# Optimization experiments

Hardware: AMD Instinct MI355X
Metric: run time of the kernel (lower is better)

Reference implementation:

```python
import jax, jax.numpy as jnp
import numpy as np

B, N, C, H, D, K = 8, 2000, 64, 64, 16, 2  # batch, nodes, hidden, hidden_hidden, embed_dim, cheb_k


def setup_inputs() -> dict:
    key = jax.random.key(0)
    ks = jax.random.split(key, 12)
    f = lambda k, s, sc=1.0: jax.random.normal(k, s, dtype=jnp.float32) * sc
    return {
        "z": f(ks[0], (B, N, C)),
        "W_in": f(ks[1], (H, C), 0.1),
        "b_in": f(ks[2], (H,), 0.1),
        "W_out": f(ks[3], (C * C, H), 0.05),
        "b_out": f(ks[4], (C * C,), 0.05),
        "emb": f(ks[5], (N, D), 0.1),
        "wp": f(ks[6], (D, K, H, H), 0.1),
        "bp": f(ks[7], (D, H), 0.1),
        "w1": f(ks[8], (C,)),
        "w2": f(ks[9], (C,)),
        "vs": f(ks[10], (N, N), 0.02),
        "bs": f(ks[11], (N, N), 0.02),
    }


def reference(z, W_in, b_in, W_out, b_out, emb, wp, bp, w1, w2, vs, bs):
    # linear_in + relu: (B,N,C) -> (B,N,H)
    h = jax.nn.relu(jnp.einsum("bnc,hc->bnh", z, W_in) + b_in)

    # data-adaptive graph: softmax over rows of relu(emb @ emb^T)
    A = jax.nn.softmax(jax.nn.relu(emb @ emb.T), axis=1)  # (N,N)
    S = jnp.stack([jnp.eye(N, dtype=z.dtype), A], axis=0)  # (K,N,N), cheb_k=2

    # spatial attention on h (x = h.unsqueeze(1), f_in == H == C)
    e1 = h @ w1  # (B,N)
    e2 = h @ w2  # (B,N)
    prod = e1[:, :, None] * e2[:, None, :]  # (B,N,N) outer product
    E = jax.nn.softmax(
        jnp.einsum("nm,bmp->bnp", vs, jax.nn.sigmoid(prod + bs)), axis=-1
    )  # (B,N,N)

    # batched supports: E.unsqueeze(1) @ S -> (B,K,N,N)
    sup = jnp.einsum("bnm,kmp->bknp", E, S)

    # node-adaptive weights / bias
    weights = jnp.einsum("nd,dkio->nkio", emb, wp)  # (N,K,H,H)
    bias = emb @ bp  # (N,H)

    # graph conv
    x_g = jnp.einsum("bknm,bmc->bnkc", sup, h)  # (B,N,K,H)
    g = jnp.einsum("bnki,nkio->bno", x_g, weights) + bias  # (B,N,H)

    # linear_out + view + tanh, scaled by 0.1
    out = jnp.tanh(jnp.einsum("bnh,oh->bno", g, W_out) + b_out)
    return 0.1 * out.reshape(B, N, C, C)
```

## Files before the change

### kernel.cpp

```cpp
#include <hip/hip_runtime.h>
#include <hip/hip_bf16.h>

#define NN 2000
#define NP 2048
#define BB 8
#define HH 64
#define DD 16

typedef __hip_bfloat16 bf16;
typedef short bf16x8 __attribute__((ext_vector_type(8)));
typedef float f32x4 __attribute__((ext_vector_type(4)));

__device__ __forceinline__ float fast_sigmoid(float x) {
    return 1.0f / (1.0f + __expf(-x));
}
__device__ __forceinline__ float fast_tanh(float x) {
    float e = __expf(2.0f * x);
    return 1.0f - 2.0f / (e + 1.0f);
}

__device__ __forceinline__ void glds16(const void* g, void* l) {
    __builtin_amdgcn_global_load_lds(
        (const __attribute__((address_space(1))) void*)g,
        (__attribute__((address_space(3))) void*)l, 16, 0, 0);
}

__global__ __launch_bounds__(256) void k_h(
        const float* __restrict__ z, const float* __restrict__ W_in,
        const float* __restrict__ b_in, const float* __restrict__ w1,
        const float* __restrict__ w2, float* __restrict__ h,
        float* __restrict__ e1, float* __restrict__ e2) {
    __shared__ float WT[64 * 65];
    __shared__ float zs[4][64];
    int t = threadIdx.x;
    int lane = t & 63, ty = t >> 6;
    int bn0 = blockIdx.x * 4;
    for (int i = t; i < 64 * 64; i += 256) {
        int hh = i >> 6, c = i & 63;
        WT[c * 65 + hh] = W_in[i];
    }
    zs[ty][lane] = z[(size_t)(bn0 + ty) * 64 + lane];
    __syncthreads();
    float acc = b_in[lane];
    #pragma unroll
    for (int c = 0; c < 64; c++) acc += zs[ty][c] * WT[c * 65 + lane];
    float hv = fmaxf(acc, 0.0f);
    h[(size_t)(bn0 + ty) * 64 + lane] = hv;
    float p1 = hv * w1[lane], p2 = hv * w2[lane];
    #pragma unroll
    for (int off = 32; off > 0; off >>= 1) {
        p1 += __shfl_down(p1, off);
        p2 += __shfl_down(p2, off);
    }
    if (lane == 0) { e1[bn0 + ty] = p1; e2[bn0 + ty] = p2; }
}

__global__ __launch_bounds__(256) void k_mega(
        const float* __restrict__ e1, const float* __restrict__ e2,
        const float* __restrict__ bs, bf16* __restrict__ Tt,
        const float* __restrict__ vs, bf16* __restrict__ vs_bf,
        const float* __restrict__ emb, bf16* __restrict__ A,
        const float* __restrict__ wp, float* __restrict__ Wn_all,
        const float* __restrict__ h, bf16* __restrict__ hTcat,
        bf16* __restrict__ hsT,
        const float* __restrict__ W_out, bf16* __restrict__ Wo_bf) {
    __shared__ float smem[4160];
    int bid = blockIdx.x, t = threadIdx.x;

    if (bid < 8192) {
        int b = bid >> 10, rem = bid & 1023;
        int mt = rem & 31, pt = rem >> 5;
        const float* e1b = e1 + (size_t)b * NN;
        const float* e2b = e2 + (size_t)b * NN;
        bf16* Tb = Tt + (size_t)b * NP * NP;
        float* tile = smem;
        int tx = t & 63, ty = t >> 6;
        int m0 = mt * 64, p0 = pt * 64;
        int p = p0 + tx;
        float e2v = (p < NN) ? e2b[p] : 0.0f;
        for (int i = ty * 16; i < ty * 16 + 16; i++) {
            int m = m0 + i;
            float v = 0.0f;
            if (m < NN && p < NN)
                v = fast_sigmoid(e1b[m] * e2v + bs[(size_t)m * NN + p]);
            tile[i * 65 + tx] = v;
        }
        __syncthreads();
        for (int i = ty * 16; i < ty * 16 + 16; i++)
            Tb[((size_t)p0 + i) * NP + m0 + tx] =
                __float2bfloat16(tile[tx * 65 + i]);
        return;
    }
    bid -= 8192;
    if (bid < 16384) {
        int id = bid * 256 + t;
        int n = id >> 11, m = id & (NP - 1);
        float v = (n < NN && m < NN) ? vs[n * NN + m] : 0.0f;
        vs_bf[id] = __float2bfloat16(v);
        return;
    }
    bid -= 16384;
    if (bid < 2048) {
        int i = bid;
        if (i >= NN) {
            for (int j = t; j < NP; j += 256) A[(size_t)i * NP + j] = __float2bfloat16(0.0f);
            return;
        }
        float* rowbuf = smem;
        float* red = smem + 2048;
        float* ei = smem + 2304;
        if (t < DD) ei[t] = emb[i * DD + t];
        __syncthreads();
        float lmax = -1e30f;
        for (int j = t; j < NP; j += 256) {
            float s = 0.0f;
            if (j < NN) {
                #pragma unroll
                for (int d = 0; d < DD; d++) s += ei[d] * emb[j * DD + d];
                s = fmaxf(s, 0.0f);
                lmax = fmaxf(lmax, s);
            }
            rowbuf[j] = s;
        }
        red[t] = lmax; __syncthreads();
        for (int o = 128; o > 0; o >>= 1) { if (t < o) red[t] = fmaxf(red[t], red[t + o]); __syncthreads(); }
        float mx = red[0];
        __syncthreads();
        float lsum = 0.0f;
        for (int j = t; j < NN; j += 256) {
            float e = __expf(rowbuf[j] - mx);
            rowbuf[j] = e; lsum += e;
        }
        red[t] = lsum; __syncthreads();
        for (int o = 128; o > 0; o >>= 1) { if (t < o) red[t] += red[t + o]; __syncthreads(); }
        float inv = 1.0f / red[0];
        for (int j = t; j < NP; j += 256)
            A[(size_t)i * NP + j] = __float2bfloat16(j < NN ? rowbuf[j] * inv : 0.0f);
        return;
    }
    bid -= 2048;
    if (bid < 512) {
        float* embs = smem;
        int n0 = (bid & 15) * 128;
        int jo = (bid >> 4) * 256 + t;
        float wv[16];
        #pragma unroll
        for (int d = 0; d < 16; d++) wv[d] = wp[(size_t)d * 8192 + jo];
        for (int s = t; s < 128 * 16; s += 256) {
            int i = s >> 4, d = s & 15;
            int n = n0 + i;
            embs[s] = (n < NN) ? emb[n * 16 + d] : 0.f;
        }
        __syncthreads();
        for (int i = 0; i < 128; i++) {
            int n = n0 + i;
            if (n >= NN) break;
            const f32x4* ev = (const f32x4*)&embs[i * 16];
            f32x4 ea = ev[0], eb = ev[1], ec = ev[2], ed = ev[3];
            float a = 0.f;
            #pragma unroll
            for (int q = 0; q < 4; q++) a += ea[q] * wv[q];
            #pragma unroll
            for (int q = 0; q < 4; q++) a += eb[q] * wv[4 + q];
            #pragma unroll
            for (int q = 0; q < 4; q++) a += ec[q] * wv[8 + q];
            #pragma unroll
            for (int q = 0; q < 4; q++) a += ed[q] * wv[12 + q];
            Wn_all[(size_t)n * 8192 + jo] = a;
        }
        return;
    }
    bid -= 512;
    if (bid < 256) {
        float* tile = smem;
        int nt = bid & 31, b = bid >> 5;
        int tx = t & 63, ty = t >> 6;
        int n0 = nt * 64;
        for (int i = ty * 16; i < ty * 16 + 16; i++) {
            int n = n0 + i;
            tile[i * 65 + tx] = (n < NN) ? h[((size_t)b * NN + n) * 64 + tx] : 0.0f;
        }
        __syncthreads();
        for (int i = ty * 16; i < ty * 16 + 16; i++) {
            bf16 v = __float2bfloat16(tile[tx * 65 + i]);
            hTcat[((size_t)b * 64 + i) * NP + n0 + tx] = v;
            hsT[((size_t)b * 128 + i) * NP + n0 + tx] = v;
        }
        return;
    }
    bid -= 256;
    {
        int id = bid * 256 + t;
        Wo_bf[id] = __float2bfloat16(W_out[id]);
    }
}

__global__ __launch_bounds__(256) void k_redT(const float* __restrict__ AhPart,
                                              bf16* __restrict__ hsT) {
    __shared__ float tile[64 * 65];
    int pt = blockIdx.x, b = blockIdx.y;
    int tx = threadIdx.x & 63, ty = threadIdx.x >> 6;
    int p0 = pt * 64, q0 = b * 64;
    const long long TOT = (long long)NP * 512;
    for (int i = ty * 16; i < ty * 16 + 16; i++) {
        long long base = ((long long)p0 + i) * 512 + q0 + tx;
        float s = AhPart[base];
        #pragma unroll
        for (int sl = 1; sl < 4; sl++) s += AhPart[sl * TOT + base];
        tile[i * 65 + tx] = s;
    }
    __syncthreads();
    for (int i = ty * 16; i < ty * 16 + 16; i++)
        hsT[((size_t)b * 128 + 64 + i) * NP + p0 + tx] =
            __float2bfloat16(tile[tx * 65 + i]);
}

__global__ __launch_bounds__(512, 4) void k_gemm256pv(
        const bf16* __restrict__ X, const bf16* __restrict__ Yt,
        const bf16* __restrict__ hsT, float* __restrict__ xgPart,
        float* __restrict__ rsPart,
        int K, int ldx, int ldy, long long sY, long long sHs) {
    __shared__ short LDSb[32768];
    short* Asb = LDSb;
    short* Bsb = LDSb + 8192;
    int bx = blockIdx.x, by = blockIdx.y, z = blockIdx.z;
    const bf16* Xp = X;
    const bf16* Yp = Yt + (long long)z * sY;
    int tid = threadIdx.x;
    int m0 = bx * 128, n0 = by * 256;
    int wave = tid >> 6, lane = tid & 63;
    int wr = wave >> 2, wc = wave & 3;
    int fr = lane & 15, kq = lane >> 4;

    f32x4 zero = {0.f, 0.f, 0.f, 0.f};
    f32x4 acc[4][4];
    #pragma unroll
    for (int i = 0; i < 4; i++)
        #pragma unroll
        for (int j = 0; j < 4; j++) acc[i][j] = zero;

    int r4 = tid >> 2, slot = tid & 3;
    int scol = (slot ^ ((r4 >> 1) & 3)) * 8;
    const bf16* xsrc = Xp + (long long)(m0 + r4) * ldx + scol;
    const bf16* ysrc = Yp + (long long)(n0 + r4) * ldy + scol;
    short* Ad = Asb + tid * 8;
    short* Bd = Bsb + tid * 8;

    auto STAGE = [&](int tile) {
        int bufA = (tile & 1) * 4096;
        int bufB = (tile & 1) * 8192;
        long long ko = (long long)tile * 32;
        glds16(xsrc + ko, Ad + bufA);
        glds16(ysrc + ko, Bd + bufB);
        glds16(ysrc + 128 * (long long)ldy + ko, Bd + bufB + 4096);
    };

    int aoff[4], boff[4];
    #pragma unroll
    for (int i = 0; i < 4; i++) {
        int row = wr * 64 + i * 16 + fr;
        aoff[i] = row * 32 + ((kq ^ ((row >> 1) & 3)) << 3);
    }
    #pragma unroll
    for (int j = 0; j < 4; j++) {
        int row = wc * 64 + j * 16 + fr;
        boff[j] = row * 32 + ((kq ^ ((row >> 1) & 3)) << 3);
    }

    int NT = K >> 5;
    STAGE(0); STAGE(1);
    asm volatile("s_waitcnt vmcnt(3)" ::: "memory");
    __builtin_amdgcn_s_barrier();

    for (int t = 0; t < NT; t++) {
        const short* Ab = Asb + (t & 1) * 4096;
        const short* Bb = Bsb + (t & 1) * 8192;
        bf16x8 a[4], b[4];
        #pragma unroll
        for (int i = 0; i < 4; i++) a[i] = *(const bf16x8*)(Ab + aoff[i]);
        #pragma unroll
        for (int j = 0; j < 4; j++) b[j] = *(const bf16x8*)(Bb + boff[j]);
        __builtin_amdgcn_s_setprio(1);
        #pragma unroll
        for (int i = 0; i < 4; i++)
            #pragma unroll
            for (int j = 0; j < 4; j++)
                acc[i][j] = __builtin_amdgcn_mfma_f32_16x16x32_bf16(a[i], b[j], acc[i][j], 0, 0, 0);
        __builtin_amdgcn_s_setprio(0);
        __builtin_amdgcn_sched_barrier(0);
        __builtin_amdgcn_s_barrier();
        __builtin_amdgcn_sched_barrier(0);
        if (t + 2 < NT) {
            STAGE(t + 2);
            asm volatile("s_waitcnt vmcnt(3)" ::: "memory");
        } else if (t + 1 < NT) {
            asm volatile("s_waitcnt vmcnt(0)" ::: "memory");
        }
        __builtin_amdgcn_s_barrier();
    }
    __syncthreads();

    int rq = kq * 4;
    #pragma unroll
    for (int i = 0; i < 4; i++) {
        #pragma unroll
        for (int r = 0; r < 4; r++) {
            int lrow = wr * 64 + i * 16 + rq + r;
            float rs = 0.f;
            #pragma unroll
            for (int j = 0; j < 4; j++) {
                int lcol = wc * 64 + j * 16 + fr;
                float e = (n0 + lcol < NN) ? __expf(acc[i][j][r]) : 0.f;
                bf16 bv = __float2bfloat16(e);
                int sl = (lcol >> 3) ^ (lrow & 7);
                LDSb[lrow * 256 + sl * 8 + (lcol & 7)] = *(short*)&bv;
                rs += e;
            }
            rs += __shfl_xor(rs, 1);
            rs += __shfl_xor(rs, 2);
            rs += __shfl_xor(rs, 4);
            rs += __shfl_xor(rs, 8);
            if (fr == 0)
                rsPart[((long long)z * 32 + by * 4 + wc) * NP + m0 + lrow] = rs;
        }
    }
    __syncthreads();

    const bf16* hz = hsT + (long long)z * sHs;
    int wr2 = wave >> 2, wc2 = wave & 3;
    f32x4 acc2[4][2];
    #pragma unroll
    for (int i = 0; i < 4; i++)
        #pragma unroll
        for (int jj = 0; jj < 2; jj++) acc2[i][jj] = zero;
    #pragma unroll
    for (int ks = 0; ks < 8; ks++) {
        bf16x8 a2[4], b2[2];
        #pragma unroll
        for (int i = 0; i < 4; i++) {
            int row = wr2 * 64 + i * 16 + fr;
            int sl = (ks * 4 + kq) ^ (row & 7);
            a2[i] = *(const bf16x8*)(LDSb + row * 256 + sl * 8);
        }
        #pragma unroll
        for (int jj = 0; jj < 2; jj++)
            b2[jj] = *(const bf16x8*)(hz + (long long)(wc2 * 32 + jj * 16 + fr) * NP
                                      + n0 + ks * 32 + kq * 8);
        #pragma unroll
        for (int i = 0; i < 4; i++)
            #pragma unroll
            for (int jj = 0; jj < 2; jj++)
                acc2[i][jj] = __builtin_amdgcn_mfma_f32_16x16x32_bf16(a2[i], b2[jj], acc2[i][jj], 0, 0, 0);
    }
    #pragma unroll
    for (int i = 0; i < 4; i++)
        #pragma unroll
        for (int jj = 0; jj < 2; jj++) {
            int jcol = wc2 * 32 + jj * 16 + fr;
            #pragma unroll
            for (int r = 0; r < 4; r++) {
                int n = m0 + wr2 * 64 + i * 16 + rq + r;
                xgPart[(long long)n * 8192 + by * 1024 + z * 128 + jcol] = acc2[i][jj][r];
            }
        }
}

template<bool TANH, int KSPLIT>
__global__ __launch_bounds__(256) void k_gemm_bt(
        const bf16* __restrict__ X, const bf16* __restrict__ Yt,
        float* __restrict__ C, const float* __restrict__ bias,
        int K, int ldx, int ldy, int ldc,
        long long sX, long long sY, long long sC, long long sSlice) {
    __shared__ short As[128 * 32];
    __shared__ short Bs[128 * 32];
    int zz = blockIdx.z;
    int ks = 0;
    if (KSPLIT > 1) { ks = zz % KSPLIT; zz /= KSPLIT; }
    const bf16* Xp = X + (long long)zz * sX;
    const bf16* Yp = Yt + (long long)zz * sY;
    float* Cp = C + (long long)zz * sC + (long long)ks * sSlice;
    int tid = threadIdx.x;
    int m0 = blockIdx.x * 128, n0 = blockIdx.y * 128;
    int wave = tid >> 6, lane = tid & 63;
    int wm = (wave >> 1) * 64, wn = (wave & 1) * 64;
    int fr = lane & 15, kq = lane >> 4;

    f32x4 zero = {0.f, 0.f, 0.f, 0.f};
    f32x4 acc[4][4];
    #pragma unroll
    for (int i = 0; i < 4; i++)
        #pragma unroll
        for (int j = 0; j < 4; j++) acc[i][j] = zero;

    int lrow = lane >> 2, lcol = (lane & 3) * 8;
    const bf16* xg0 = Xp + (long long)(m0 + wave * 16 + lrow) * ldx + lcol;
    const bf16* xg1 = xg0 + (long long)64 * ldx;
    const bf16* yg0 = Yp + (long long)(n0 + wave * 16 + lrow) * ldy + lcol;
    const bf16* yg1 = yg0 + (long long)64 * ldy;
    short* lA0 = As + wave * 512;
    short* lA1 = As + (wave + 4) * 512;
    short* lB0 = Bs + wave * 512;
    short* lB1 = Bs + (wave + 4) * 512;

    int kbeg = (KSPLIT > 1) ? ks * (K / KSPLIT) : 0;
    int kend = kbeg + K / KSPLIT;
    for (int k0 = kbeg; k0 < kend; k0 += 32) {
        __syncthreads();
        glds16(xg0 + k0, lA0);
        glds16(xg1 + k0, lA1);
        glds16(yg0 + k0, lB0);
        glds16(yg1 + k0, lB1);
        __syncthreads();
        bf16x8 a[4], b[4];
        #pragma unroll
        for (int i = 0; i < 4; i++)
            a[i] = *(const bf16x8*)(As + (wm + i * 16 + fr) * 32 + kq * 8);
        #pragma unroll
        for (int j = 0; j < 4; j++)
            b[j] = *(const bf16x8*)(Bs + (wn + j * 16 + fr) * 32 + kq * 8);
        #pragma unroll
        for (int i = 0; i < 4; i++)
            #pragma unroll
            for (int j = 0; j < 4; j++)
                acc[i][j] = __builtin_amdgcn_mfma_f32_16x16x32_bf16(a[i], b[j], acc[i][j], 0, 0, 0);
    }
    int rq = kq * 4;
    for (int i = 0; i < 4; i++)
        for (int j = 0; j < 4; j++) {
            int col = n0 + wn + j * 16 + fr;
            float bv = TANH ? bias[col] : 0.0f;
            #pragma unroll
            for (int r = 0; r < 4; r++) {
                int row = m0 + wm + i * 16 + rq + r;
                float v = acc[i][j][r];
                Cp[(long long)row * ldc + col] =
                    TANH ? 0.1f * fast_tanh(v + bv) : v;
            }
        }
}

__global__ __launch_bounds__(256) void k_g(
        const float* __restrict__ Wn_all, const float* __restrict__ bp,
        const float* __restrict__ emb, const float* __restrict__ xgPart,
        const float* __restrict__ rsPart, bf16* __restrict__ gbf) {
    __shared__ float Wn[8192];
    __shared__ float xgs[1024];
    __shared__ float biass[64];
    __shared__ float invs[8];
    __shared__ float rsred[256];
    int n = blockIdx.x, t = threadIdx.x;
    rsred[t] = rsPart[(size_t)t * NP + n];
    if (t >= 64 && t < 128) {
        int o = t - 64;
        float a = 0.f;
        #pragma unroll
        for (int d = 0; d < 16; d++) a += emb[n * 16 + d] * bp[d * 64 + o];
        biass[o] = a;
    }
    {
        const f32x4* src = (const f32x4*)(Wn_all + (size_t)n * 8192);
        f32x4* dst = (f32x4*)Wn;
        #pragma unroll
        for (int s = 0; s < 8; s++) dst[s * 256 + t] = src[s * 256 + t];
    }
    __syncthreads();
    if (t < 8) {
        float s = 0.f;
        #pragma unroll
        for (int y = 0; y < 32; y++) s += rsred[t * 32 + y];
        invs[t] = 1.0f / s;
    }
    __syncthreads();
    for (int s = 0; s < 4; s++) {
        int id = t + s * 256;
        int b = id >> 7, j = id & 127;
        const float* xp = xgPart + (size_t)n * 8192 + b * 128 + j;
        float a = xp[0];
        #pragma unroll
        for (int by = 1; by < 8; by++) a += xp[by * 1024];
        xgs[id] = a * invs[b];
    }
    __syncthreads();
    int o = t & 63, bh = t >> 6;
    for (int half = 0; half < 2; half++) {
        int b = bh + half * 4;
        float a = biass[o];
        for (int j = 0; j < 128; j++) a += xgs[b * 128 + j] * Wn[j * 64 + o];
        gbf[((size_t)b * NN + n) * 64 + o] = __float2bfloat16(a);
    }
}

extern "C" void kernel_launch(void* const* d_in, const int* in_sizes, int n_in,
                              void* d_out, int out_size, void* d_ws, size_t ws_size,
                              hipStream_t stream) {
    const float* z     = (const float*)d_in[0];
    const float* W_in  = (const float*)d_in[1];
    const float* b_in  = (const float*)d_in[2];
    const float* W_out = (const float*)d_in[3];
    const float* b_out = (const float*)d_in[4];
    const float* emb   = (const float*)d_in[5];
    const float* wp    = (const float*)d_in[6];
    const float* bp    = (const float*)d_in[7];
    const float* w1    = (const float*)d_in[8];
    const float* w2    = (const float*)d_in[9];
    const float* vs    = (const float*)d_in[10];
    const float* bs    = (const float*)d_in[11];

    char* p = (char*)d_ws;
    auto alloc = [&](size_t bytes) -> char* {
        char* r = p;
        p += (bytes + 255) & ~(size_t)255;
        return r;
    };
    float* h       = (float*)alloc((size_t)BB * NN * 64 * 4);
    float* e1      = (float*)alloc((size_t)BB * NN * 4);
    float* e2      = (float*)alloc((size_t)BB * NN * 4);
    bf16*  A_bf    = (bf16*) alloc((size_t)NP * NP * 2);
    bf16*  vs_bf   = (bf16*) alloc((size_t)NP * NP * 2);
    bf16*  Tt_all  = (bf16*) alloc((size_t)BB * NP * NP * 2);
    float* rsPart  = (float*)alloc((size_t)BB * 32 * NP * 4);
    bf16*  hTcat   = (bf16*) alloc((size_t)512 * NP * 2);
    float* AhPart  = (float*)alloc((size_t)4 * NP * 512 * 4);
    bf16*  hsT     = (bf16*) alloc((size_t)BB * 128 * NP * 2);
    float* xgPart  = (float*)alloc((size_t)NP * 8192 * 4);
    bf16*  gbf     = (bf16*) alloc((size_t)BB * NN * 64 * 2);
    bf16*  Wo_bf   = (bf16*) alloc((size_t)4096 * 64 * 2);
    float* Wn_all  = (float*)alloc((size_t)NN * 8192 * 4);

    k_h<<<BB * NN / 4, 256, 0, stream>>>(z, W_in, b_in, w1, w2, h, e1, e2);

    k_mega<<<8192 + 16384 + 2048 + 512 + 256 + 1024, 256, 0, stream>>>(
        e1, e2, bs, Tt_all, vs, vs_bf, emb, A_bf, wp, Wn_all,
        h, hTcat, hsT, W_out, Wo_bf);

    k_gemm_bt<false, 4><<<dim3(16, 4, 4), 256, 0, stream>>>(
        A_bf, hTcat, AhPart, nullptr, NP, NP, NP, 512,
        0, 0, 0, (long long)NP * 512);
    k_redT<<<dim3(NP / 64, BB), 256, 0, stream>>>(AhPart, hsT);

    k_gemm256pv<<<dim3(16, 8, BB), 512, 0, stream>>>(
        vs_bf, Tt_all, hsT, xgPart, rsPart, NP, NP, NP,
        (long long)NP * NP, (long long)128 * NP);

    k_g<<<NN, 256, 0, stream>>>(Wn_all, bp, emb, xgPart, rsPart, gbf);
    k_gemm_bt<true, 1><<<dim3(125, 32, 1), 256, 0, stream>>>(
        gbf, Wo_bf, (float*)d_out, b_out, 64, 64, 64, 4096, 0, 0, 0, 0);
}
```

Measured before the change: 620.3 us.

## Enlarge fused vs@T GEMM tile to 256x256 with 8-phase k64 pipeline

The fused softmax-numerator GEMM plus PV kernel now uses a 256x256 output tile per block instead of 128x256, which halves the grid in x and doubles A/B reuse per staged tile. The main loop is rebuilt as an 8-phase software pipeline over 64-wide K steps with double-buffered halves, finer-grained global-to-LDS staging, vmcnt-based waits and a new XOR swizzle. This uses 128KB of LDS and far more accumulator registers, dropping occupancy to 2 blocks per CU. The grid falls to 512 blocks, which may fill the CUs less evenly.

```diff
diff --git a/kernel.cpp b/kernel.cpp
--- a/kernel.cpp
+++ b/kernel.cpp
@@ -215,97 +215,124 @@
             __float2bfloat16(tile[tx * 65 + i]);
 }
 
-__global__ __launch_bounds__(512, 4) void k_gemm256pv(
+#define MFMA_B16 __builtin_amdgcn_mfma_f32_16x16x32_bf16
+#define VM8 asm volatile("s_waitcnt vmcnt(8)" ::: "memory")
+#define VM4 asm volatile("s_waitcnt vmcnt(4)" ::: "memory")
+#define VM0 asm volatile("s_waitcnt vmcnt(0)" ::: "memory")
+#define VMN
+#define PHASE(BUF, KH, JP, READA, STAGE, VMS)                                \
+  {                                                                          \
+    if (READA) {                                                             \
+      _Pragma("unroll")                                                      \
+      for (int ii = 0; ii < 8; ii++)                                         \
+        a[ii] = *(const bf16x8*)(LDSb + (BUF) * 16384 + (KH) * 8192 + aoff[ii]); \
+    }                                                                        \
+    b[0] = *(const bf16x8*)(LDSb + 32768 + (BUF) * 16384 + (KH) * 8192 + boff[(JP) * 2]); \
+    b[1] = *(const bf16x8*)(LDSb + 32768 + (BUF) * 16384 + (KH) * 8192 + boff[(JP) * 2 + 1]); \
+    STAGE;                                                                   \
+    asm volatile("s_waitcnt lgkmcnt(0)" ::: "memory");                       \
+    __builtin_amdgcn_sched_barrier(0);                                       \
+    __builtin_amdgcn_s_setprio(1);                                           \
+    _Pragma("unroll")                                                        \
+    for (int ii = 0; ii < 8; ii++) {                                         \
+      acc[ii][(JP) * 2]     = MFMA_B16(a[ii], b[0], acc[ii][(JP) * 2], 0, 0, 0);     \
+      acc[ii][(JP) * 2 + 1] = MFMA_B16(a[ii], b[1], acc[ii][(JP) * 2 + 1], 0, 0, 0); \
+    }                                                                        \
+    __builtin_amdgcn_s_setprio(0);                                           \
+    __builtin_amdgcn_sched_barrier(0);                                       \
+    VMS;                                                                     \
+    __builtin_amdgcn_s_barrier();                                            \
+    __builtin_amdgcn_sched_barrier(0);                                       \
+  }
+
+__global__ __launch_bounds__(512, 2) void k_gemm256pv(
         const bf16* __restrict__ X, const bf16* __restrict__ Yt,
         const bf16* __restrict__ hsT, float* __restrict__ xgPart,
         float* __restrict__ rsPart,
         int K, int ldx, int ldy, long long sY, long long sHs) {
-    __shared__ short LDSb[32768];
-    short* Asb = LDSb;
-    short* Bsb = LDSb + 8192;
+    __shared__ short LDSb[65536];
     int bx = blockIdx.x, by = blockIdx.y, z = blockIdx.z;
     const bf16* Xp = X;
     const bf16* Yp = Yt + (long long)z * sY;
     int tid = threadIdx.x;
-    int m0 = bx * 128, n0 = by * 256;
+    int m0 = bx * 256, n0 = by * 256;
     int wave = tid >> 6, lane = tid & 63;
     int wr = wave >> 2, wc = wave & 3;
     int fr = lane & 15, kq = lane >> 4;
 
     f32x4 zero = {0.f, 0.f, 0.f, 0.f};
-    f32x4 acc[4][4];
-    #pragma unroll
-    for (int i = 0; i < 4; i++)
+    f32x4 acc[8][4];
+    #pragma unroll
+    for (int i = 0; i < 8; i++)
         #pragma unroll
         for (int j = 0; j < 4; j++) acc[i][j] = zero;
 
-    int r4 = tid >> 2, slot = tid & 3;
-    int scol = (slot ^ ((r4 >> 1) & 3)) * 8;
-    const bf16* xsrc = Xp + (long long)(m0 + r4) * ldx + scol;
-    const bf16* ysrc = Yp + (long long)(n0 + r4) * ldy + scol;
-    short* Ad = Asb + tid * 8;
-    short* Bd = Bsb + tid * 8;
-
-    auto STAGE = [&](int tile) {
-        int bufA = (tile & 1) * 4096;
-        int bufB = (tile & 1) * 8192;
-        long long ko = (long long)tile * 32;
-        glds16(xsrc + ko, Ad + bufA);
-        glds16(ysrc + ko, Bd + bufB);
-        glds16(ysrc + 128 * (long long)ldy + ko, Bd + bufB + 4096);
+    auto SR = [&](int isA, int buf, int kh, int tile) {
+        int rbase = (isA ? 0 : 32768) + buf * 16384 + kh * 8192;
+        long long kb = (long long)tile * 64 + kh * 32;
+        #pragma unroll
+        for (int q = 0; q < 2; q++) {
+            int pos = q * 512 + tid;
+            int row = pos >> 2;
+            int scol = ((pos & 3) ^ (row & 3) ^ ((row >> 2) & 3)) * 8;
+            const bf16* g = (isA ? Xp + (long long)(m0 + row) * ldx
+                                 : Yp + (long long)(n0 + row) * ldy) + kb + scol;
+            glds16(g, LDSb + rbase + pos * 8);
+        }
     };
 
-    int aoff[4], boff[4];
-    #pragma unroll
-    for (int i = 0; i < 4; i++) {
-        int row = wr * 64 + i * 16 + fr;
-        aoff[i] = row * 32 + ((kq ^ ((row >> 1) & 3)) << 3);
+    int aoff[8], boff[4];
+    #pragma unroll
+    for (int i = 0; i < 8; i++) {
+        int row = wr * 128 + i * 16 + fr;
+        aoff[i] = row * 32 + ((kq ^ (row & 3) ^ ((row >> 2) & 3)) << 3);
     }
     #pragma unroll
     for (int j = 0; j < 4; j++) {
         int row = wc * 64 + j * 16 + fr;
-        boff[j] = row * 32 + ((kq ^ ((row >> 1) & 3)) << 3);
-    }
-
-    int NT = K >> 5;
-    STAGE(0); STAGE(1);
-    asm volatile("s_waitcnt vmcnt(3)" ::: "memory");
+        boff[j] = row * 32 + ((kq ^ (row & 3) ^ ((row >> 2) & 3)) << 3);
+    }
+
+    bf16x8 a[8], b[2];
+    int NITER = K >> 7;
+
+    SR(1, 0, 0, 0); SR(0, 0, 0, 0);
+    SR(1, 0, 1, 0); SR(0, 0, 1, 0);
+    SR(1, 1, 0, 1); SR(0, 1, 0, 1);
+    VM8;
     __builtin_amdgcn_s_barrier();
-
-    for (int t = 0; t < NT; t++) {
-        const short* Ab = Asb + (t & 1) * 4096;
-        const short* Bb = Bsb + (t & 1) * 8192;
-        bf16x8 a[4], b[4];
-        #pragma unroll
-        for (int i = 0; i < 4; i++) a[i] = *(const bf16x8*)(Ab + aoff[i]);
-        #pragma unroll
-        for (int j = 0; j < 4; j++) b[j] = *(const bf16x8*)(Bb + boff[j]);
-        __builtin_amdgcn_s_setprio(1);
-        #pragma unroll
-        for (int i = 0; i < 4; i++)
-            #pragma unroll
-            for (int j = 0; j < 4; j++)
-                acc[i][j] = __builtin_amdgcn_mfma_f32_16x16x32_bf16(a[i], b[j], acc[i][j], 0, 0, 0);
-        __builtin_amdgcn_s_setprio(0);
-        __builtin_amdgcn_sched_barrier(0);
-        __builtin_amdgcn_s_barrier();
-        __builtin_amdgcn_sched_barrier(0);
-        if (t + 2 < NT) {
-            STAGE(t + 2);
-            asm volatile("s_waitcnt vmcnt(3)" ::: "memory");
-        } else if (t + 1 < NT) {
-            asm volatile("s_waitcnt vmcnt(0)" ::: "memory");
-        }
-        __builtin_amdgcn_s_barrier();
+    __builtin_amdgcn_sched_barrier(0);
+
+    for (int i = 0; i < NITER - 1; i++) {
+        int t1 = 2 * i + 1, t2 = 2 * i + 2, t3 = 2 * i + 3;
+        PHASE(0, 0, 0, 1, { SR(1, 1, 1, t1); }, VM8)
+        PHASE(0, 0, 1, 0, { SR(0, 1, 1, t1); }, VM8)
+        PHASE(0, 1, 0, 1, { SR(1, 0, 0, t2); }, VM8)
+        PHASE(0, 1, 1, 0, { SR(0, 0, 0, t2); }, VM8)
+        PHASE(1, 0, 0, 1, { SR(1, 0, 1, t2); }, VM8)
+        PHASE(1, 0, 1, 0, { SR(0, 0, 1, t2); }, VM8)
+        PHASE(1, 1, 0, 1, { SR(1, 1, 0, t3); }, VM8)
+        PHASE(1, 1, 1, 0, { SR(0, 1, 0, t3); }, VM8)
+    }
+    {
+        int t1 = 2 * NITER - 1;
+        PHASE(0, 0, 0, 1, { SR(1, 1, 1, t1); }, VM8)
+        PHASE(0, 0, 1, 0, { SR(0, 1, 1, t1); }, VM8)
+        PHASE(0, 1, 0, 1, { }, VM8)
+        PHASE(0, 1, 1, 0, { }, VM4)
+        PHASE(1, 0, 0, 1, { }, VM4)
+        PHASE(1, 0, 1, 0, { }, VM0)
+        PHASE(1, 1, 0, 1, { }, VMN)
+        PHASE(1, 1, 1, 0, { }, VMN)
     }
     __syncthreads();
 
     int rq = kq * 4;
     #pragma unroll
-    for (int i = 0; i < 4; i++) {
+    for (int i = 0; i < 8; i++) {
         #pragma unroll
         for (int r = 0; r < 4; r++) {
-            int lrow = wr * 64 + i * 16 + rq + r;
+            int lrow = wr * 128 + i * 16 + rq + r;
             float rs = 0.f;
             #pragma unroll
             for (int j = 0; j < 4; j++) {
@@ -328,17 +355,17 @@
 
     const bf16* hz = hsT + (long long)z * sHs;
     int wr2 = wave >> 2, wc2 = wave & 3;
-    f32x4 acc2[4][2];
-    #pragma unroll
-    for (int i = 0; i < 4; i++)
+    f32x4 acc2[8][2];
+    #pragma unroll
+    for (int i = 0; i < 8; i++)
         #pragma unroll
         for (int jj = 0; jj < 2; jj++) acc2[i][jj] = zero;
     #pragma unroll
     for (int ks = 0; ks < 8; ks++) {
-        bf16x8 a2[4], b2[2];
-        #pragma unroll
-        for (int i = 0; i < 4; i++) {
-            int row = wr2 * 64 + i * 16 + fr;
+        bf16x8 a2[8], b2[2];
+        #pragma unroll
+        for (int i = 0; i < 8; i++) {
+            int row = wr2 * 128 + i * 16 + fr;
             int sl = (ks * 4 + kq) ^ (row & 7);
             a2[i] = *(const bf16x8*)(LDSb + row * 256 + sl * 8);
         }
@@ -347,19 +374,19 @@
             b2[jj] = *(const bf16x8*)(hz + (long long)(wc2 * 32 + jj * 16 + fr) * NP
                                       + n0 + ks * 32 + kq * 8);
         #pragma unroll
-        for (int i = 0; i < 4; i++)
+        for (int i = 0; i < 8; i++)
             #pragma unroll
             for (int jj = 0; jj < 2; jj++)
-                acc2[i][jj] = __builtin_amdgcn_mfma_f32_16x16x32_bf16(a2[i], b2[jj], acc2[i][jj], 0, 0, 0);
-    }
-    #pragma unroll
-    for (int i = 0; i < 4; i++)
+                acc2[i][jj] = MFMA_B16(a2[i], b2[jj], acc2[i][jj], 0, 0, 0);
+    }
+    #pragma unroll
+    for (int i = 0; i < 8; i++)
         #pragma unroll
         for (int jj = 0; jj < 2; jj++) {
             int jcol = wc2 * 32 + jj * 16 + fr;
             #pragma unroll
             for (int r = 0; r < 4; r++) {
-                int n = m0 + wr2 * 64 + i * 16 + rq + r;
+                int n = m0 + wr2 * 128 + i * 16 + rq + r;
                 xgPart[(long long)n * 8192 + by * 1024 + z * 128 + jcol] = acc2[i][jj][r];
             }
         }
@@ -538,7 +565,7 @@
         0, 0, 0, (long long)NP * 512);
     k_redT<<<dim3(NP / 64, BB), 256, 0, stream>>>(AhPart, hsT);
 
-    k_gemm256pv<<<dim3(16, 8, BB), 512, 0, stream>>>(
+    k_gemm256pv<<<dim3(8, 8, BB), 512, 0, stream>>>(
         vs_bf, Tt_all, hsT, xgPart, rsPart, NP, NP, NP,
         (long long)NP * NP, (long long)128 * NP);
 
```

After: 609.0 us. About the same (-1.8%).
